# Performance work log

Measured on AMD Instinct MI355X. Metric: run time of the kernel, lower is better.

Reference implementation:

```python
import jax, jax.numpy as jnp
from jax import lax
import numpy as np

T = 36
N_POLES = 161
GAMMA = 0.05
MAX_ITER = 40


def creat_real_dictionary(T, rr, theta):
    # i = 0..T-1 power/frequency index
    i = jnp.arange(T, dtype=rr.dtype)[:, None]            # [T,1]
    ri = rr[None, :] ** i                                  # rr^i, [T,N]
    sgn = jnp.where(jnp.arange(T)[:, None] % 2 == 0, 1.0, -1.0).astype(rr.dtype)
    nri = sgn * ri                                         # (-rr)^i
    c = jnp.cos(i * theta[None, :])
    s = jnp.sin(i * theta[None, :])
    ones = jnp.ones((T, 1), rr.dtype)
    dic = jnp.concatenate([ones, ri * c, nri * c, ri * s, nri * s], axis=1)  # [T, 4N+1]
    G = jnp.linalg.norm(dic, axis=0)                       # column norms
    G = jnp.where(G == 0, jnp.sqrt(jnp.asarray(T, rr.dtype)), G)
    return dic / G


def fista(D, Y, gamma, max_iter):
    DtD = D.T @ D                                          # [K,K]
    L = jnp.linalg.norm(DtD)                               # Frobenius norm (torch.norm(., p=2))
    linv = jnp.where(L == 0, 0.0, 1.0 / L)
    DtY = jnp.einsum('tk,btp->bkp', D, Y) * linv           # [B,K,P]
    lambd = gamma * linv                                   # scalar
    A = jnp.eye(DtD.shape[0], dtype=D.dtype) - DtD * linv  # [K,K]

    # momentum coefficients are data-independent -> precompute on host
    t = 1.0
    tts = []
    for _ in range(max_iter):
        t_new = (1 + np.sqrt(1 + 4 * t * t)) / 2.0
        tts.append((t - 1) / t_new)
        t = t_new
    tts = jnp.asarray(np.asarray(tts, dtype=np.float32))

    x0 = jnp.zeros(DtY.shape, dtype=D.dtype)

    def step(carry, tt):
        x_old, y_old = carry
        Ay = jnp.einsum('kj,bjp->bkp', A, y_old)
        x_new = Ay + DtY - lambd
        # faithful to source: sign(x) * max(|x|, 0)
        x_new = jnp.sign(x_new) * jnp.maximum(jnp.abs(x_new), 0.0)
        y_new = x_new * (1 + tt) - x_old * tt
        return (x_new, y_new), None

    (x_final, _), _ = lax.scan(step, (x0, x0), tts)
    return x_final


def setup_inputs() -> dict:
    key = jax.random.key(0)
    k1, k2, k3 = jax.random.split(key, 3)
    B, P = 1, 8192
    x = jax.random.normal(k1, (B, T, P), dtype=jnp.float32)
    # pole radii near unit circle, angles in [0, pi]
    rr = 0.85 + 0.3 * jax.random.uniform(k2, (N_POLES,), dtype=jnp.float32)
    theta = np.pi * jax.random.uniform(k3, (N_POLES,), dtype=jnp.float32)
    return {"x": x, "rr": rr, "theta": theta}


def reference(x, rr, theta):
    dic = creat_real_dictionary(T, rr, theta)
    return fista(dic, x, GAMMA, MAX_ITER)
```

## Files before the change

kernel.cpp:

```cpp
#include <hip/hip_runtime.h>
#include <math.h>

#define T36   36
#define NPOLE 161
#define K645  645
#define KH    37
#define NITER 40
#define GAMMA_C 0.05


__global__ void k_build_dict(const float* __restrict__ rr, const float* __restrict__ theta,
                             double* __restrict__ Dt) {
    int k = blockIdx.x * blockDim.x + threadIdx.x;
    if (k >= K645) return;
    if (k == 0) {
        const double inv = 1.0 / 6.0;
        for (int i = 0; i < T36; ++i) Dt[i] = inv;
        return;
    }
    int g = (k - 1) / NPOLE;
    int p = (k - 1) % NPOLE;
    double r  = (double)rr[p];
    double th = (double)theta[p];
    bool alt     = (g == 1) || (g == 3);
    bool use_sin = (g >= 2);
    double ss = 0.0, rp = 1.0;
    for (int i = 0; i < T36; ++i) {
        double s, c;
        sincos(th * (double)i, &s, &c);
        double v = rp * (use_sin ? s : c);
        if (alt && (i & 1)) v = -v;
        ss += v * v;
        rp *= r;
    }
    double gn = sqrt(ss);
    if (gn == 0.0) gn = 6.0;
    double inv = 1.0 / gn;
    rp = 1.0;
    for (int i = 0; i < T36; ++i) {
        double s, c;
        sincos(th * (double)i, &s, &c);
        double v = rp * (use_sin ? s : c);
        if (alt && (i & 1)) v = -v;
        Dt[k * T36 + i] = v * inv;
        rp *= r;
    }
}

__global__ void k_gram(const double* __restrict__ Dt, double* __restrict__ G36,
                       double* __restrict__ d1v) {
    int a = blockIdx.x;
    int b = blockIdx.y;
    int lane = threadIdx.x;
    double acc = 0.0;
    if (b < T36) {
        for (int k = lane; k < K645; k += 64) acc += Dt[k * T36 + a] * Dt[k * T36 + b];
    } else {
        for (int k = lane; k < K645; k += 64) acc += Dt[k * T36 + a];
    }
    for (int off = 32; off > 0; off >>= 1) acc += __shfl_down(acc, off);
    if (lane == 0) {
        if (b < T36) G36[a * T36 + b] = acc;
        else         d1v[a] = acc;
    }
}

__global__ void k_finalize(const double* __restrict__ G36, const double* __restrict__ d1v,
                           double* __restrict__ scal, double* __restrict__ H) {
    int tid = threadIdx.x;
    double s = 0.0;
    for (int i = tid; i < T36 * T36; i += 1024) { double v = G36[i]; s += v * v; }
    for (int off = 32; off > 0; off >>= 1) s += __shfl_down(s, off);
    __shared__ double wsum[16];
    __shared__ double sc[2];
    if ((tid & 63) == 0) wsum[tid >> 6] = s;
    __syncthreads();
    if (tid == 0) {
        double tot = 0.0;
        for (int w = 0; w < 16; ++w) tot += wsum[w];
        double L = sqrt(tot);
        double linv = (L == 0.0) ? 0.0 : 1.0 / L;
        sc[0] = linv;
        sc[1] = GAMMA_C * linv;
        scal[0] = sc[0];
        scal[1] = sc[1];
    }
    __syncthreads();
    double linv = sc[0];
    for (int idx = tid; idx < KH * KH; idx += 1024) {
        int a = idx / KH, q = idx % KH;
        double h;
        if (a < T36) h = ((a == q) ? 1.0 : 0.0) - linv * ((q < T36) ? G36[a * T36 + q] : d1v[a]);
        else         h = (q == T36) ? 1.0 : 0.0;
        H[idx] = h;
    }
}

__global__ void k_iterate(const double* __restrict__ H, const double* __restrict__ scal,
                          double* __restrict__ Ufin) {
    int t = blockIdx.x;
    int lane = threadIdx.x;
    __shared__ double yl[KH];
    double Hreg[KH];
    double Eh = 0.0, xold = 0.0;
    double linv = scal[0], lambd = scal[1];
    if (lane < KH) {
#pragma unroll
        for (int q = 0; q < KH; ++q) Hreg[q] = H[lane * KH + q];
        Eh = (lane < T36) ? ((lane == t && t < T36) ? linv : 0.0)
                          : ((t == T36) ? -lambd : 0.0);
        yl[lane] = 0.0;
    } else {
#pragma unroll
        for (int q = 0; q < KH; ++q) Hreg[q] = 0.0;
    }
    __syncthreads();
    double tcur = 1.0;
    for (int n = 0; n < NITER; ++n) {
        double tn = 0.5 * (1.0 + sqrt(1.0 + 4.0 * tcur * tcur));
        double tt = (double)(float)((tcur - 1.0) / tn);
        tcur = tn;
        double acc = Eh;
#pragma unroll
        for (int q = 0; q < KH; ++q) acc += Hreg[q] * yl[q];
        __syncthreads();
        double ynew = (1.0 + tt) * acc - tt * xold;
        xold = acc;
        if (lane < KH) yl[lane] = ynew;
        __syncthreads();
    }
    if (lane < KH) Ufin[lane * KH + t] = xold;
}

__global__ void k_expand(const double* __restrict__ Dt, const double* __restrict__ Ufin,
                         float* __restrict__ Mf) {
    int idx = blockIdx.x * 256 + threadIdx.x;
    if (idx >= K645 * KH) return;
    int k = idx / KH, t = idx % KH;
    double acc = Ufin[T36 * KH + t];
#pragma unroll
    for (int q = 0; q < T36; ++q) acc += Dt[k * T36 + q] * Ufin[q * KH + t];
    Mf[idx] = (float)acc;
}

__global__ __launch_bounds__(256) void k_out(const float* __restrict__ Y,
                                             const float* __restrict__ Mf,
                                             float* __restrict__ out, int P) {
    int p = blockIdx.x * 256 + threadIdx.x;
    if (p >= P) return;
    int k0 = blockIdx.y * 15;
    float y[T36];
#pragma unroll
    for (int t = 0; t < T36; ++t) y[t] = Y[t * P + p];
    for (int kk = 0; kk < 15; ++kk) {
        int k = k0 + kk;
        const float* m = Mf + k * KH;
        float acc = m[T36];
#pragma unroll
        for (int t = 0; t < T36; ++t) acc = fmaf(m[t], y[t], acc);
        out[k * P + p] = acc;
    }
}

extern "C" void kernel_launch(void* const* d_in, const int* in_sizes, int n_in,
                              void* d_out, int out_size, void* d_ws, size_t ws_size,
                              hipStream_t stream) {
    const float* x     = (const float*)d_in[0];
    const float* rr    = (const float*)d_in[1];
    const float* theta = (const float*)d_in[2];
    float* out = (float*)d_out;

    double* ws   = (double*)d_ws;
    double* Dt   = ws;
    double* G36  = ws + 23220;
    double* d1v  = ws + 24516;
    double* scal = ws + 24552;
    double* H    = ws + 24554;
    double* Ufin = ws + 25923;
    float*  Mf   = (float*)(ws + 27292);

    int P = in_sizes[0] / T36;

    k_build_dict<<<dim3((K645 + 255) / 256), dim3(256), 0, stream>>>(rr, theta, Dt);
    k_gram<<<dim3(T36, KH), dim3(64), 0, stream>>>(Dt, G36, d1v);
    k_finalize<<<dim3(1), dim3(1024), 0, stream>>>(G36, d1v, scal, H);
    k_iterate<<<dim3(KH), dim3(64), 0, stream>>>(H, scal, Ufin);
    k_expand<<<dim3((K645 * KH + 255) / 256), dim3(256), 0, stream>>>(Dt, Ufin, Mf);
    k_out<<<dim3((P + 255) / 256, 43), dim3(256), 0, stream>>>(x, Mf, out, P);
}
```

Baseline: 126.4 us.

## Fuse finalize/iterate/expand into one solve kernel and transpose dictionary layout

Merges the norm/H construction, the FISTA recurrence and the expansion into the output matrix into a single kernel, cutting the launch count from six to four. The dictionary is now stored time-major so the gram and expand loops read it with coalesced accesses. The dictionary build replaces 72 per-element sincos calls with an angle-addition recurrence and keeps values in registers. The matvec in the iteration splits its accumulation into two chains to shorten the dependency. Each solve block now recomputes the Frobenius norm redundantly, and the recurrence can drift slightly from direct sincos.

After: 110.4 us. 1.14x faster.

```diff
diff --git a/kernel.cpp b/kernel.cpp
--- a/kernel.cpp
+++ b/kernel.cpp
@@ -9,13 +9,14 @@
 #define GAMMA_C 0.05
 
 
-__global__ void k_build_dict(const float* __restrict__ rr, const float* __restrict__ theta,
-                             double* __restrict__ Dt) {
+__global__ void k_build(const float* __restrict__ rr, const float* __restrict__ theta,
+                        double* __restrict__ Di) {
     int k = blockIdx.x * blockDim.x + threadIdx.x;
     if (k >= K645) return;
     if (k == 0) {
         const double inv = 1.0 / 6.0;
-        for (int i = 0; i < T36; ++i) Dt[i] = inv;
+#pragma unroll
+        for (int i = 0; i < T36; ++i) Di[i * K645] = inv;
         return;
     }
     int g = (k - 1) / NPOLE;
@@ -24,40 +25,42 @@
     double th = (double)theta[p];
     bool alt     = (g == 1) || (g == 3);
     bool use_sin = (g >= 2);
-    double ss = 0.0, rp = 1.0;
+    double sth, cth;
+    sincos(th, &sth, &cth);
+    double ci = 1.0, si = 0.0, rp = 1.0, ss = 0.0;
+    double val[T36];
+#pragma unroll
     for (int i = 0; i < T36; ++i) {
-        double s, c;
-        sincos(th * (double)i, &s, &c);
-        double v = rp * (use_sin ? s : c);
+        double v = rp * (use_sin ? si : ci);
         if (alt && (i & 1)) v = -v;
+        val[i] = v;
         ss += v * v;
-        rp *= r;
+        double cn = ci * cth - si * sth;
+        double sn = si * cth + ci * sth;
+        ci = cn; si = sn; rp *= r;
     }
     double gn = sqrt(ss);
     if (gn == 0.0) gn = 6.0;
     double inv = 1.0 / gn;
-    rp = 1.0;
-    for (int i = 0; i < T36; ++i) {
-        double s, c;
-        sincos(th * (double)i, &s, &c);
-        double v = rp * (use_sin ? s : c);
-        if (alt && (i & 1)) v = -v;
-        Dt[k * T36 + i] = v * inv;
-        rp *= r;
-    }
+#pragma unroll
+    for (int i = 0; i < T36; ++i) Di[i * K645 + k] = val[i] * inv;
 }
 
-__global__ void k_gram(const double* __restrict__ Dt, double* __restrict__ G36,
-                       double* __restrict__ d1v) {
+__global__ __launch_bounds__(64) void k_gram(const double* __restrict__ Di,
+                                             double* __restrict__ G36,
+                                             double* __restrict__ d1v) {
     int a = blockIdx.x;
     int b = blockIdx.y;
     int lane = threadIdx.x;
+    const double* Da = Di + a * K645;
     double acc = 0.0;
     if (b < T36) {
-        for (int k = lane; k < K645; k += 64) acc += Dt[k * T36 + a] * Dt[k * T36 + b];
+        const double* Db = Di + b * K645;
+        for (int k = lane; k < K645; k += 64) acc += Da[k] * Db[k];
     } else {
-        for (int k = lane; k < K645; k += 64) acc += Dt[k * T36 + a];
+        for (int k = lane; k < K645; k += 64) acc += Da[k];
     }
+#pragma unroll
     for (int off = 32; off > 0; off >>= 1) acc += __shfl_down(acc, off);
     if (lane == 0) {
         if (b < T36) G36[a * T36 + b] = acc;
@@ -65,50 +68,36 @@
     }
 }
 
-__global__ void k_finalize(const double* __restrict__ G36, const double* __restrict__ d1v,
-                           double* __restrict__ scal, double* __restrict__ H) {
-    int tid = threadIdx.x;
-    double s = 0.0;
-    for (int i = tid; i < T36 * T36; i += 1024) { double v = G36[i]; s += v * v; }
-    for (int off = 32; off > 0; off >>= 1) s += __shfl_down(s, off);
-    __shared__ double wsum[16];
-    __shared__ double sc[2];
-    if ((tid & 63) == 0) wsum[tid >> 6] = s;
-    __syncthreads();
-    if (tid == 0) {
-        double tot = 0.0;
-        for (int w = 0; w < 16; ++w) tot += wsum[w];
-        double L = sqrt(tot);
-        double linv = (L == 0.0) ? 0.0 : 1.0 / L;
-        sc[0] = linv;
-        sc[1] = GAMMA_C * linv;
-        scal[0] = sc[0];
-        scal[1] = sc[1];
-    }
-    __syncthreads();
-    double linv = sc[0];
-    for (int idx = tid; idx < KH * KH; idx += 1024) {
-        int a = idx / KH, q = idx % KH;
-        double h;
-        if (a < T36) h = ((a == q) ? 1.0 : 0.0) - linv * ((q < T36) ? G36[a * T36 + q] : d1v[a]);
-        else         h = (q == T36) ? 1.0 : 0.0;
-        H[idx] = h;
-    }
-}
-
-__global__ void k_iterate(const double* __restrict__ H, const double* __restrict__ scal,
-                          double* __restrict__ Ufin) {
+__global__ __launch_bounds__(64) void k_solve(const double* __restrict__ Di,
+                                              const double* __restrict__ G36,
+                                              const double* __restrict__ d1v,
+                                              float* __restrict__ Mf) {
     int t = blockIdx.x;
     int lane = threadIdx.x;
-    __shared__ double yl[KH];
+    double s = 0.0;
+    for (int i = lane; i < T36 * T36; i += 64) { double v = G36[i]; s += v * v; }
+#pragma unroll
+    for (int off = 32; off > 0; off >>= 1) s += __shfl_xor(s, off);
+    double L = sqrt(s);
+    double linv = (L == 0.0) ? 0.0 : 1.0 / L;
+    double lambd = GAMMA_C * linv;
+
     double Hreg[KH];
     double Eh = 0.0, xold = 0.0;
-    double linv = scal[0], lambd = scal[1];
+    __shared__ double yl[KH];
+    __shared__ double xl[KH];
     if (lane < KH) {
+        if (lane < T36) {
 #pragma unroll
-        for (int q = 0; q < KH; ++q) Hreg[q] = H[lane * KH + q];
-        Eh = (lane < T36) ? ((lane == t && t < T36) ? linv : 0.0)
-                          : ((t == T36) ? -lambd : 0.0);
+            for (int q = 0; q < T36; ++q)
+                Hreg[q] = ((lane == q) ? 1.0 : 0.0) - linv * G36[lane * T36 + q];
+            Hreg[T36] = -linv * d1v[lane];
+            Eh = (lane == t && t < T36) ? linv : 0.0;
+        } else {
+#pragma unroll
+            for (int q = 0; q < KH; ++q) Hreg[q] = (q == T36) ? 1.0 : 0.0;
+            Eh = (t == T36) ? -lambd : 0.0;
+        }
         yl[lane] = 0.0;
     } else {
 #pragma unroll
@@ -120,27 +109,27 @@
         double tn = 0.5 * (1.0 + sqrt(1.0 + 4.0 * tcur * tcur));
         double tt = (double)(float)((tcur - 1.0) / tn);
         tcur = tn;
-        double acc = Eh;
+        double a0 = Eh, a1 = 0.0;
 #pragma unroll
-        for (int q = 0; q < KH; ++q) acc += Hreg[q] * yl[q];
+        for (int q = 0; q < T36; q += 2) {
+            a0 += Hreg[q] * yl[q];
+            a1 += Hreg[q + 1] * yl[q + 1];
+        }
+        double acc = a0 + a1 + Hreg[T36] * yl[T36];
         __syncthreads();
         double ynew = (1.0 + tt) * acc - tt * xold;
         xold = acc;
         if (lane < KH) yl[lane] = ynew;
         __syncthreads();
     }
-    if (lane < KH) Ufin[lane * KH + t] = xold;
-}
-
-__global__ void k_expand(const double* __restrict__ Dt, const double* __restrict__ Ufin,
-                         float* __restrict__ Mf) {
-    int idx = blockIdx.x * 256 + threadIdx.x;
-    if (idx >= K645 * KH) return;
-    int k = idx / KH, t = idx % KH;
-    double acc = Ufin[T36 * KH + t];
+    if (lane < KH) xl[lane] = xold;
+    __syncthreads();
+    for (int k = lane; k < K645; k += 64) {
+        double acc = xl[T36];
 #pragma unroll
-    for (int q = 0; q < T36; ++q) acc += Dt[k * T36 + q] * Ufin[q * KH + t];
-    Mf[idx] = (float)acc;
+        for (int q = 0; q < T36; ++q) acc += Di[q * K645 + k] * xl[q];
+        Mf[k * KH + t] = (float)acc;
+    }
 }
 
 __global__ __launch_bounds__(256) void k_out(const float* __restrict__ Y,
@@ -171,20 +160,15 @@
     float* out = (float*)d_out;
 
     double* ws   = (double*)d_ws;
-    double* Dt   = ws;
+    double* Di   = ws;
     double* G36  = ws + 23220;
     double* d1v  = ws + 24516;
-    double* scal = ws + 24552;
-    double* H    = ws + 24554;
-    double* Ufin = ws + 25923;
-    float*  Mf   = (float*)(ws + 27292);
+    float*  Mf   = (float*)(ws + 24552);
 
     int P = in_sizes[0] / T36;
 
-    k_build_dict<<<dim3((K645 + 255) / 256), dim3(256), 0, stream>>>(rr, theta, Dt);
-    k_gram<<<dim3(T36, KH), dim3(64), 0, stream>>>(Dt, G36, d1v);
-    k_finalize<<<dim3(1), dim3(1024), 0, stream>>>(G36, d1v, scal, H);
-    k_iterate<<<dim3(KH), dim3(64), 0, stream>>>(H, scal, Ufin);
-    k_expand<<<dim3((K645 * KH + 255) / 256), dim3(256), 0, stream>>>(Dt, Ufin, Mf);
+    k_build<<<dim3((K645 + 255) / 256), dim3(256), 0, stream>>>(rr, theta, Di);
+    k_gram<<<dim3(T36, KH), dim3(64), 0, stream>>>(Di, G36, d1v);
+    k_solve<<<dim3(KH), dim3(64), 0, stream>>>(Di, G36, d1v, Mf);
     k_out<<<dim3((P + 255) / 256, 43), dim3(256), 0, stream>>>(x, Mf, out, P);
 }
```
